# Optimization experiments

Hardware: AMD Instinct MI355X
Metric: run time of the kernel (lower is better)

The kernel has to match this reference:

```python
import jax, jax.numpy as jnp
import numpy as np


def _cell(x, ch_sum, cc_sum, W, b):
    # gates = W @ [child_h_sum, x] + b ; chunk order: f, i, c_tilde, o
    gates = jnp.concatenate([ch_sum, x], axis=-1) @ W.T + b
    f, i, ct, o = jnp.split(gates, 4, axis=-1)
    c = jax.nn.sigmoid(f) * cc_sum + jax.nn.sigmoid(i) * jnp.tanh(ct)
    h = jax.nn.sigmoid(o) * jnp.tanh(c)
    return h, c


def setup_inputs() -> dict:
    key = jax.random.key(0)
    k1, k2 = jax.random.split(key)
    H = 128                       # hidden_size == input_size (forced by recursion)
    L = 2 ** 17                   # num leaves of a perfect binary tree
    leaf_features = jax.random.normal(k1, (L, H), dtype=jnp.float32)
    lim = float(np.sqrt(6.0 / (2 * H + 4 * H)))  # xavier_uniform for (4H, 2H)
    W = jax.random.uniform(k2, (4 * H, 2 * H), minval=-lim, maxval=lim, dtype=jnp.float32)
    b = jnp.zeros((4 * H,), dtype=jnp.float32)
    return {"leaf_features": leaf_features, "W": W, "b": b}


def reference(leaf_features, W, b):
    H = W.shape[0] // 4
    L = leaf_features.shape[0]
    # Leaf level: no children -> child_h_sum = child_c_sum = 0
    zeros = jnp.zeros((L, H), dtype=leaf_features.dtype)
    h, c = _cell(leaf_features, zeros, zeros, W, b)
    # Internal levels (perfect binary tree), bottom-up. Loop count is static
    # (log2(L) levels), each iteration is fully vectorized over the level.
    while h.shape[0] > 1:
        hl, hr = h[0::2], h[1::2]
        cl, cr = c[0::2], c[1::2]
        ch_sum = hl + hr            # sum(child_h)
        x = ch_sum * 0.5            # child_h_avg (mean over 2 children)
        cc_sum = cl + cr            # summed child cell states
        h, c = _cell(x, ch_sum, cc_sum, W, b)
    return h  # root hidden state, shape (1, H)
```

## Files before the change

kernel.cpp:

```cpp
#include <hip/hip_runtime.h>

#define HH 128
#define NT 512
#define PT 256

typedef float  f32x4  __attribute__((ext_vector_type(4)));
typedef _Float16 f16x8 __attribute__((ext_vector_type(8)));

static __device__ __forceinline__ unsigned int pk16(float a, float b){
  unsigned short ha = __builtin_bit_cast(unsigned short, (_Float16)a);
  unsigned short hb = __builtin_bit_cast(unsigned short, (_Float16)b);
  return (unsigned int)ha | ((unsigned int)hb << 16);
}
static __device__ __forceinline__ float f16_to_f(unsigned short s){
  return (float)__builtin_bit_cast(_Float16, s);
}

__device__ __forceinline__ float sigf(float x){
  float t = __builtin_amdgcn_exp2f(-1.44269504089f * x);
  return __builtin_amdgcn_rcpf(1.f + t);
}
__device__ __forceinline__ float tanhf_(float x){
  float t = __builtin_amdgcn_exp2f(2.88539008178f * x);
  return 1.f - 2.f*__builtin_amdgcn_rcpf(t + 1.f);
}

__global__ __launch_bounds__(PT) void prep_pack(
    const float* __restrict__ W,
    unsigned short* __restrict__ pE, unsigned short* __restrict__ pL)
{
  int idx = blockIdx.x*PT + threadIdx.x;
  int l  = idx & 63;
  int kc = (idx >> 6) & 3;
  int gl = (idx >> 8) & 7;
  int wp = (idx >> 11);
  int q  = gl >> 1, ft = gl & 1;
  int g  = q*128 + wp*32 + ft*16 + (l & 15);
  int kbase = kc*32 + (l >> 4)*8;

  unsigned short ev[8], lv[8];
#pragma unroll
  for (int j = 0; j < 8; ++j){
    int k = kbase + j;
    float w0 = W[g*256 + k];
    float w1 = W[g*256 + 128 + k];
    float we = w0 + 0.5f*w1;
    ev[j] = __builtin_bit_cast(unsigned short, (_Float16)we);
    lv[j] = __builtin_bit_cast(unsigned short, (_Float16)w1);
  }
  long base = (long)idx*8;
  *(f16x8*)&pE[base] = *(f16x8*)ev;
  *(f16x8*)&pL[base] = *(f16x8*)lv;
}

__global__ __launch_bounds__(NT, 2) void leafK(
    const float* __restrict__ x_leaf,
    const unsigned short* __restrict__ pL,
    const float* __restrict__ bias,
    unsigned short* __restrict__ HpO,
    float* __restrict__ csO, int ntiles)
{
  __shared__ unsigned short AsH[2][32*HH];

  const int t = threadIdx.x, w = t>>6, l = t&63;
  const int a = l>>4, fcol = l&15, feat = w*16 + fcol;

  f16x8 rb[3][4];
#pragma unroll
  for (int qq = 0; qq < 3; ++qq)
#pragma unroll
    for (int kc = 0; kc < 4; ++kc){
      long off = ((long)((((w>>1)*8) + (qq+1)*2 + (w&1))*4 + kc)*64 + l)*8;
      rb[qq][kc] = *(const f16x8*)&pL[off];
    }
  const float Bi = bias[HH + feat], Bg = bias[2*HH + feat], Bo = bias[3*HH + feat];

  const int srow = t>>4, sci = t&15;
  float sv[8];
  auto sload = [&](int tile){
    long base = ((long)tile*32 + srow)*HH + sci*8;
    *(float4*)&sv[0] = *(const float4*)&x_leaf[base];
    *(float4*)&sv[4] = *(const float4*)&x_leaf[base+4];
  };
  auto swrite = [&](int buf){
    unsigned int hp[4];
#pragma unroll
    for (int p = 0; p < 4; ++p) hp[p] = pk16(sv[2*p], sv[2*p+1]);
    uint4 hq = {hp[0],hp[1],hp[2],hp[3]};
    int off = srow*256 + ((sci*16) ^ ((srow&7)<<4));
    *(uint4*)((char*)&AsH[buf][0] + off) = hq;
  };

  int tile = blockIdx.x;
  if (tile < ntiles){ sload(tile); swrite(0); }
  __syncthreads();
  int buf = 0;

  for (; tile < ntiles; tile += gridDim.x){
#pragma unroll
    for (int qq = 0; qq < 3; ++qq)
#pragma unroll
      for (int kc = 0; kc < 4; ++kc)
        asm volatile("" : "+v"(rb[qq][kc]));

    int nxt = tile + gridDim.x;
    bool have = nxt < ntiles;
    if (have) sload(nxt);

    f32x4 acc[2][3];
#pragma unroll
    for (int mt = 0; mt < 2; ++mt)
#pragma unroll
      for (int qq = 0; qq < 3; ++qq) acc[mt][qq] = (f32x4)(0.f);

#pragma unroll
    for (int kc = 0; kc < 4; ++kc){
      f16x8 aH[2];
#pragma unroll
      for (int mt = 0; mt < 2; ++mt){
        int row = mt*16 + fcol;
        int off = row*256 + ((kc*64 + a*16) ^ ((row&7)<<4));
        aH[mt] = *(const f16x8*)((const char*)&AsH[buf][0] + off);
      }
#pragma unroll
      for (int qq = 0; qq < 3; ++qq)
#pragma unroll
        for (int mt = 0; mt < 2; ++mt)
          acc[mt][qq] = __builtin_amdgcn_mfma_f32_16x16x32_f16(aH[mt], rb[qq][kc], acc[mt][qq], 0, 0, 0);
    }

#pragma unroll
    for (int mt = 0; mt < 2; ++mt){
      float hv[4], cv[4];
#pragma unroll
      for (int rr = 0; rr < 4; ++rr){
        float iv = acc[mt][0][rr] + Bi;
        float gv = acc[mt][1][rr] + Bg;
        float ov = acc[mt][2][rr] + Bo;
        float c = sigf(iv)*tanhf_(gv);
        float h = sigf(ov)*tanhf_(c);
        hv[rr] = h; cv[rr] = c;
      }
#pragma unroll
      for (int p = 0; p < 2; ++p){
        long prow = (long)tile*16 + mt*8 + a*2 + p;
        float hs = hv[2*p] + hv[2*p+1];
        HpO[prow*HH + feat] = __builtin_bit_cast(unsigned short, (_Float16)hs);
        csO[prow*HH + feat] = cv[2*p] + cv[2*p+1];
      }
    }

    if (have) swrite(buf^1);
    __syncthreads();
    buf ^= 1;
  }
}

__global__ __launch_bounds__(NT, 2) void fuse2(
    const unsigned short* __restrict__ hPH,
    const float* __restrict__ cP,
    const unsigned short* __restrict__ pE,
    const float* __restrict__ bias,
    unsigned short* __restrict__ HpO,
    float* __restrict__ csO, int ntiles)
{
  __shared__ unsigned short AsH[2][32*HH];
  __shared__ float HsF[16*HH];
  __shared__ float CsF[16*HH];

  const int t = threadIdx.x, w = t>>6, l = t&63;
  const int a = l>>4, fcol = l&15, feat = w*16 + fcol;

  f16x8 rb[4][4];
#pragma unroll
  for (int q = 0; q < 4; ++q)
#pragma unroll
    for (int kc = 0; kc < 4; ++kc){
      long off = ((long)((((w>>1)*8) + q*2 + (w&1))*4 + kc)*64 + l)*8;
      rb[q][kc] = *(const f16x8*)&pE[off];
    }
  float B4[4];
#pragma unroll
  for (int q = 0; q < 4; ++q) B4[q] = bias[q*HH + feat];

  const int srow = t>>4, sci = t&15;
  f16x8 svH;
  auto sload = [&](int tile){
    long base = ((long)tile*32 + srow)*HH + sci*8;
    svH = *(const f16x8*)&hPH[base];
  };
  auto swrite = [&](int buf){
    int off = srow*256 + ((sci*16) ^ ((srow&7)<<4));
    *(f16x8*)((char*)&AsH[buf][0] + off) = svH;
  };

  int tile = blockIdx.x;
  if (tile < ntiles){ sload(tile); swrite(0); }
  __syncthreads();
  int buf = 0;

  for (; tile < ntiles; tile += gridDim.x){
#pragma unroll
    for (int q = 0; q < 4; ++q)
#pragma unroll
      for (int kc = 0; kc < 4; ++kc)
        asm volatile("" : "+v"(rb[q][kc]));

    int nxt = tile + gridDim.x;
    bool have = nxt < ntiles;

    float cc0[2][4];
#pragma unroll
    for (int mt = 0; mt < 2; ++mt)
#pragma unroll
      for (int rr = 0; rr < 4; ++rr)
        cc0[mt][rr] = cP[((long)tile*32 + mt*16 + a*4 + rr)*HH + feat];

    if (have) sload(nxt);

    f32x4 acc0[2][4];
#pragma unroll
    for (int mt = 0; mt < 2; ++mt)
#pragma unroll
      for (int q = 0; q < 4; ++q) acc0[mt][q] = (f32x4)(0.f);

#pragma unroll
    for (int kc = 0; kc < 4; ++kc){
      f16x8 aH[2];
#pragma unroll
      for (int mt = 0; mt < 2; ++mt){
        int row = mt*16 + fcol;
        int off = row*256 + ((kc*64 + a*16) ^ ((row&7)<<4));
        aH[mt] = *(const f16x8*)((const char*)&AsH[buf][0] + off);
      }
#pragma unroll
      for (int q = 0; q < 4; ++q)
#pragma unroll
        for (int mt = 0; mt < 2; ++mt)
          acc0[mt][q] = __builtin_amdgcn_mfma_f32_16x16x32_f16(aH[mt], rb[q][kc], acc0[mt][q], 0, 0, 0);
    }

#pragma unroll
    for (int mt = 0; mt < 2; ++mt){
      float hv[4], cv[4];
#pragma unroll
      for (int rr = 0; rr < 4; ++rr){
        float fv = acc0[mt][0][rr] + B4[0];
        float iv = acc0[mt][1][rr] + B4[1];
        float gv = acc0[mt][2][rr] + B4[2];
        float ov = acc0[mt][3][rr] + B4[3];
        float c = sigf(fv)*cc0[mt][rr] + sigf(iv)*tanhf_(gv);
        float h = sigf(ov)*tanhf_(c);
        hv[rr] = h; cv[rr] = c;
      }
#pragma unroll
      for (int p = 0; p < 2; ++p){
        int row1 = mt*8 + a*2 + p;
        int o1 = row1*512 + ((feat*4) ^ ((row1&7)<<4));
        *(float*)((char*)HsF + o1) = hv[2*p] + hv[2*p+1];
        *(float*)((char*)CsF + o1) = cv[2*p] + cv[2*p+1];
      }
    }
    if (have) swrite(buf^1);
    __syncthreads();

    f32x4 acc1[4];
#pragma unroll
    for (int q = 0; q < 4; ++q) acc1[q] = (f32x4)(0.f);

#pragma unroll
    for (int kc = 0; kc < 4; ++kc){
      f16x8 a1H;
      {
        int cb = kc*128 + a*32;
        const char* base = (const char*)HsF + fcol*512;
        float av[8];
        *(float4*)&av[0] = *(const float4*)(base + ( cb       ^ ((fcol&7)<<4)));
        *(float4*)&av[4] = *(const float4*)(base + ((cb + 16) ^ ((fcol&7)<<4)));
        unsigned int hp[4];
#pragma unroll
        for (int p = 0; p < 4; ++p) hp[p] = pk16(av[2*p], av[2*p+1]);
        uint4 hq = {hp[0],hp[1],hp[2],hp[3]};
        a1H = *(f16x8*)&hq;
      }
#pragma unroll
      for (int q = 0; q < 4; ++q)
        acc1[q] = __builtin_amdgcn_mfma_f32_16x16x32_f16(a1H, rb[q][kc], acc1[q], 0, 0, 0);
    }

    {
      float hv[4], cv[4];
#pragma unroll
      for (int rr = 0; rr < 4; ++rr){
        int n = a*4 + rr;
        float ccv = *(const float*)((const char*)CsF + n*512 + ((feat*4) ^ ((n&7)<<4)));
        float fv = acc1[0][rr] + B4[0];
        float iv = acc1[1][rr] + B4[1];
        float gv = acc1[2][rr] + B4[2];
        float ov = acc1[3][rr] + B4[3];
        float c = sigf(fv)*ccv + sigf(iv)*tanhf_(gv);
        float h = sigf(ov)*tanhf_(c);
        hv[rr] = h; cv[rr] = c;
      }
#pragma unroll
      for (int p = 0; p < 2; ++p){
        long prow = (long)tile*8 + a*2 + p;
        float hs = hv[2*p] + hv[2*p+1];
        HpO[prow*HH + feat] = __builtin_bit_cast(unsigned short, (_Float16)hs);
        csO[prow*HH + feat] = cv[2*p] + cv[2*p+1];
      }
    }
    __syncthreads();
    buf ^= 1;
  }
}

template<int ROWS0, int NLEV, int INPLANES, int FINAL>
__global__ __launch_bounds__(NT, 2) void treeblk2(
    const unsigned short* __restrict__ Hp,
    const float* __restrict__ cs,
    const float* __restrict__ hraw, const float* __restrict__ craw,
    const unsigned short* __restrict__ pE,
    const float* __restrict__ bias,
    float* __restrict__ h_out, float* __restrict__ c_out,
    float* __restrict__ root_out)
{
  constexpr int MT = (ROWS0 >= 16) ? (ROWS0/16) : 1;
  __shared__ float Asum[ROWS0][132];
  __shared__ float Csum[ROWS0][132];

  const int t = threadIdx.x;
  const long blk = blockIdx.x;
  const int w = t >> 6, l = t & 63;
  const int a = l >> 4, fcol = l & 15, feat = w*16 + fcol;

  {
    constexpr int EPT = ROWS0*HH/NT;
    constexpr int TPR = HH/EPT;
    int row = t/TPR, c0 = (t%TPR)*EPT;
    if (INPLANES){
      long base = (blk*ROWS0 + row)*(long)HH + c0;
#pragma unroll
      for (int j = 0; j < EPT; ++j){
        Asum[row][c0+j] = f16_to_f(Hp[base+j]);
        Csum[row][c0+j] = cs[base+j];
      }
    } else {
      long g = (blk*2*ROWS0 + 2*row)*(long)HH + c0;
#pragma unroll
      for (int j = 0; j < EPT; ++j){
        Asum[row][c0+j] = hraw[g+j] + hraw[g+HH+j];
        Csum[row][c0+j] = craw[g+j] + craw[g+HH+j];
      }
    }
  }

  f16x8 rb[4][4];
#pragma unroll
  for (int q = 0; q < 4; ++q)
#pragma unroll
    for (int kc = 0; kc < 4; ++kc){
      long off = ((long)((((w>>1)*8) + q*2 + (w&1))*4 + kc)*64 + l)*8;
      rb[q][kc] = *(const f16x8*)&pE[off];
    }
  float B4[4];
#pragma unroll
  for (int q = 0; q < 4; ++q) B4[q] = bias[q*HH + feat];

  __syncthreads();

#pragma unroll
  for (int lv = 0; lv < NLEV; ++lv){
    const int rows  = ROWS0 >> lv;
    const int tiles = (rows >= 16) ? (rows/16) : 1;
    float hv[MT][4], cv[MT][4];

#pragma unroll
    for (int mt = 0; mt < MT; ++mt){
      if (mt >= tiles) continue;
      f16x8 aH[4];
#pragma unroll
      for (int kc = 0; kc < 4; ++kc){
        const float* ap = &Asum[mt*16 + fcol][kc*32 + a*8];
        float av[8];
        *(float4*)&av[0] = *(const float4*)&ap[0];
        *(float4*)&av[4] = *(const float4*)&ap[4];
        unsigned int hp[4];
#pragma unroll
        for (int p = 0; p < 4; ++p) hp[p] = pk16(av[2*p], av[2*p+1]);
        uint4 hq = {hp[0],hp[1],hp[2],hp[3]};
        aH[kc] = *(f16x8*)&hq;
      }
      f32x4 acc[4];
#pragma unroll
      for (int q = 0; q < 4; ++q) acc[q] = (f32x4)(0.f);
#pragma unroll
      for (int kc = 0; kc < 4; ++kc){
#pragma unroll
        for (int q = 0; q < 4; ++q)
          acc[q] = __builtin_amdgcn_mfma_f32_16x16x32_f16(aH[kc], rb[q][kc], acc[q], 0, 0, 0);
      }
#pragma unroll
      for (int rr = 0; rr < 4; ++rr){
        int n = mt*16 + a*4 + rr;
        float ccv = Csum[n][feat];
        float fv = acc[0][rr] + B4[0];
        float iv = acc[1][rr] + B4[1];
        float gv = acc[2][rr] + B4[2];
        float ov = acc[3][rr] + B4[3];
        float c = sigf(fv)*ccv + sigf(iv)*tanhf_(gv);
        float h = sigf(ov)*tanhf_(c);
        hv[mt][rr] = h; cv[mt][rr] = c;
      }
    }
    __syncthreads();

    if (lv < NLEV-1){
#pragma unroll
      for (int mt = 0; mt < MT; ++mt){
        if (mt >= tiles) continue;
#pragma unroll
        for (int p = 0; p < 2; ++p){
          int n0 = mt*16 + a*4 + 2*p;
          if (n0 < rows){
            int prow = n0 >> 1;
            Asum[prow][feat] = hv[mt][2*p] + hv[mt][2*p+1];
            Csum[prow][feat] = cv[mt][2*p] + cv[mt][2*p+1];
          }
        }
      }
      __syncthreads();
    } else if (FINAL){
      if (a == 0) root_out[feat] = hv[0][0];
    } else {
      if (a == 0){
        h_out[blk*HH + feat] = hv[0][0];
        c_out[blk*HH + feat] = cv[0][0];
      }
    }
  }
}

extern "C" void kernel_launch(void* const* d_in, const int* in_sizes, int n_in,
                              void* d_out, int out_size, void* d_ws, size_t ws_size,
                              hipStream_t stream){
  const float* leaf = (const float*)d_in[0];
  const float* W    = (const float*)d_in[1];
  const float* bias = (const float*)d_in[2];
  float* out = (float*)d_out;

  unsigned short* pE  = (unsigned short*)d_ws;
  unsigned short* pL  = pE + 65536;
  unsigned short* HpA = pL + 65536;
  unsigned short* HpB = HpA + (1l<<16)*HH;
  float* csA = (float*)(HpB + (1l<<14)*HH);
  float* csB = csA + (1l<<16)*HH;
  float* h32 = csB + (1l<<14)*HH;
  float* c32 = h32 + 32*HH;

  prep_pack<<<32, PT, 0, stream>>>(W, pE, pL);

  leafK<<<512, NT, 0, stream>>>(leaf, pL, bias, HpA, csA, 4096);
  fuse2<<<512, NT, 0, stream>>>(HpA, csA, pE, bias, HpB, csB, 2048);
  fuse2<<<256, NT, 0, stream>>>(HpB, csB, pE, bias, HpA, csA, 512);
  fuse2<<<128, NT, 0, stream>>>(HpA, csA, pE, bias, HpB, csB, 128);
  treeblk2<32,6,1,0><<<32, NT, 0, stream>>>(HpB, csB, nullptr, nullptr,
                                            pE, bias, h32, c32, nullptr);
  treeblk2<16,5,0,1><<<1, NT, 0, stream>>>(nullptr, nullptr, h32, c32,
                                           pE, bias, nullptr, nullptr, out);

  (void)in_sizes; (void)n_in; (void)out_size; (void)ws_size;
}
```

Measured before the change: 95.92 us.

## Fuse first internal tree level into leaf kernel and store hidden sums as fp16

The leaf kernel now computes the next tree level in the same pass. It stages the pair-summed h and c in shared memory and runs a second MFMA GEMM with the combined internal weights, which halves the intermediate written to global memory and removes one level from the later kernels. The shared hidden-sum staging in both leaf and fuse kernels becomes fp16, so the MMA operand is read directly without float-to-half repacking. The launch chain and workspace sizes shift down a level, and the final tree kernel is adapted for 8-row inputs padded to 16. In exchange the leaf kernel holds more weight registers, which may pressure occupancy.

New measurement: 98.86 us. 3.1% more time.

```diff
diff --git a/kernel.cpp b/kernel.cpp
--- a/kernel.cpp
+++ b/kernel.cpp
@@ -53,27 +53,38 @@
   *(f16x8*)&pL[base] = *(f16x8*)lv;
 }
 
-__global__ __launch_bounds__(NT, 2) void leafK(
+__global__ __launch_bounds__(NT, 2) void leaf2(
     const float* __restrict__ x_leaf,
-    const unsigned short* __restrict__ pL,
+    const unsigned short* __restrict__ pL, const unsigned short* __restrict__ pE,
     const float* __restrict__ bias,
     unsigned short* __restrict__ HpO,
     float* __restrict__ csO, int ntiles)
 {
   __shared__ unsigned short AsH[2][32*HH];
+  __shared__ unsigned short HsF[16*HH];
+  __shared__ float          CsF[16*HH];
 
   const int t = threadIdx.x, w = t>>6, l = t&63;
   const int a = l>>4, fcol = l&15, feat = w*16 + fcol;
 
-  f16x8 rb[3][4];
+  f16x8 rb0[3][4], rb1[4][4];
 #pragma unroll
   for (int qq = 0; qq < 3; ++qq)
 #pragma unroll
     for (int kc = 0; kc < 4; ++kc){
       long off = ((long)((((w>>1)*8) + (qq+1)*2 + (w&1))*4 + kc)*64 + l)*8;
-      rb[qq][kc] = *(const f16x8*)&pL[off];
-    }
-  const float Bi = bias[HH + feat], Bg = bias[2*HH + feat], Bo = bias[3*HH + feat];
+      rb0[qq][kc] = *(const f16x8*)&pL[off];
+    }
+#pragma unroll
+  for (int q = 0; q < 4; ++q)
+#pragma unroll
+    for (int kc = 0; kc < 4; ++kc){
+      long off = ((long)((((w>>1)*8) + q*2 + (w&1))*4 + kc)*64 + l)*8;
+      rb1[q][kc] = *(const f16x8*)&pE[off];
+    }
+  float B4[4];
+#pragma unroll
+  for (int q = 0; q < 4; ++q) B4[q] = bias[q*HH + feat];
 
   const int srow = t>>4, sci = t&15;
   float sv[8];
@@ -101,17 +112,22 @@
     for (int qq = 0; qq < 3; ++qq)
 #pragma unroll
       for (int kc = 0; kc < 4; ++kc)
-        asm volatile("" : "+v"(rb[qq][kc]));
+        asm volatile("" : "+v"(rb0[qq][kc]));
+#pragma unroll
+    for (int q = 0; q < 4; ++q)
+#pragma unroll
+      for (int kc = 0; kc < 4; ++kc)
+        asm volatile("" : "+v"(rb1[q][kc]));
 
     int nxt = tile + gridDim.x;
     bool have = nxt < ntiles;
     if (have) sload(nxt);
 
-    f32x4 acc[2][3];
+    f32x4 acc0[2][3];
 #pragma unroll
     for (int mt = 0; mt < 2; ++mt)
 #pragma unroll
-      for (int qq = 0; qq < 3; ++qq) acc[mt][qq] = (f32x4)(0.f);
+      for (int qq = 0; qq < 3; ++qq) acc0[mt][qq] = (f32x4)(0.f);
 
 #pragma unroll
     for (int kc = 0; kc < 4; ++kc){
@@ -126,7 +142,7 @@
       for (int qq = 0; qq < 3; ++qq)
 #pragma unroll
         for (int mt = 0; mt < 2; ++mt)
-          acc[mt][qq] = __builtin_amdgcn_mfma_f32_16x16x32_f16(aH[mt], rb[qq][kc], acc[mt][qq], 0, 0, 0);
+          acc0[mt][qq] = __builtin_amdgcn_mfma_f32_16x16x32_f16(aH[mt], rb0[qq][kc], acc0[mt][qq], 0, 0, 0);
     }
 
 #pragma unroll
@@ -134,23 +150,60 @@
       float hv[4], cv[4];
 #pragma unroll
       for (int rr = 0; rr < 4; ++rr){
-        float iv = acc[mt][0][rr] + Bi;
-        float gv = acc[mt][1][rr] + Bg;
-        float ov = acc[mt][2][rr] + Bo;
+        float iv = acc0[mt][0][rr] + B4[1];
+        float gv = acc0[mt][1][rr] + B4[2];
+        float ov = acc0[mt][2][rr] + B4[3];
         float c = sigf(iv)*tanhf_(gv);
         float h = sigf(ov)*tanhf_(c);
         hv[rr] = h; cv[rr] = c;
       }
 #pragma unroll
       for (int p = 0; p < 2; ++p){
-        long prow = (long)tile*16 + mt*8 + a*2 + p;
+        int row1 = mt*8 + a*2 + p;
+        float hs = hv[2*p] + hv[2*p+1];
+        *(unsigned short*)((char*)HsF + row1*256 + ((feat*2) ^ ((row1&7)<<4))) =
+            __builtin_bit_cast(unsigned short, (_Float16)hs);
+        *(float*)((char*)CsF + row1*512 + ((feat*4) ^ ((row1&7)<<4))) =
+            cv[2*p] + cv[2*p+1];
+      }
+    }
+    if (have) swrite(buf^1);
+    __syncthreads();
+
+    f32x4 acc1[4];
+#pragma unroll
+    for (int q = 0; q < 4; ++q) acc1[q] = (f32x4)(0.f);
+#pragma unroll
+    for (int kc = 0; kc < 4; ++kc){
+      int off = fcol*256 + ((kc*64 + a*16) ^ ((fcol&7)<<4));
+      f16x8 a1H = *(const f16x8*)((const char*)HsF + off);
+#pragma unroll
+      for (int q = 0; q < 4; ++q)
+        acc1[q] = __builtin_amdgcn_mfma_f32_16x16x32_f16(a1H, rb1[q][kc], acc1[q], 0, 0, 0);
+    }
+
+    {
+      float hv[4], cv[4];
+#pragma unroll
+      for (int rr = 0; rr < 4; ++rr){
+        int n = a*4 + rr;
+        float ccv = *(const float*)((const char*)CsF + n*512 + ((feat*4) ^ ((n&7)<<4)));
+        float fv = acc1[0][rr] + B4[0];
+        float iv = acc1[1][rr] + B4[1];
+        float gv = acc1[2][rr] + B4[2];
+        float ov = acc1[3][rr] + B4[3];
+        float c = sigf(fv)*ccv + sigf(iv)*tanhf_(gv);
+        float h = sigf(ov)*tanhf_(c);
+        hv[rr] = h; cv[rr] = c;
+      }
+#pragma unroll
+      for (int p = 0; p < 2; ++p){
+        long prow = (long)tile*8 + a*2 + p;
         float hs = hv[2*p] + hv[2*p+1];
         HpO[prow*HH + feat] = __builtin_bit_cast(unsigned short, (_Float16)hs);
         csO[prow*HH + feat] = cv[2*p] + cv[2*p+1];
       }
     }
-
-    if (have) swrite(buf^1);
     __syncthreads();
     buf ^= 1;
   }
@@ -165,8 +218,8 @@
     float* __restrict__ csO, int ntiles)
 {
   __shared__ unsigned short AsH[2][32*HH];
-  __shared__ float HsF[16*HH];
-  __shared__ float CsF[16*HH];
+  __shared__ unsigned short HsF[16*HH];
+  __shared__ float          CsF[16*HH];
 
   const int t = threadIdx.x, w = t>>6, l = t&63;
   const int a = l>>4, fcol = l&15, feat = w*16 + fcol;
@@ -256,9 +309,11 @@
 #pragma unroll
       for (int p = 0; p < 2; ++p){
         int row1 = mt*8 + a*2 + p;
-        int o1 = row1*512 + ((feat*4) ^ ((row1&7)<<4));
-        *(float*)((char*)HsF + o1) = hv[2*p] + hv[2*p+1];
-        *(float*)((char*)CsF + o1) = cv[2*p] + cv[2*p+1];
+        float hs = hv[2*p] + hv[2*p+1];
+        *(unsigned short*)((char*)HsF + row1*256 + ((feat*2) ^ ((row1&7)<<4))) =
+            __builtin_bit_cast(unsigned short, (_Float16)hs);
+        *(float*)((char*)CsF + row1*512 + ((feat*4) ^ ((row1&7)<<4))) =
+            cv[2*p] + cv[2*p+1];
       }
     }
     if (have) swrite(buf^1);
@@ -267,22 +322,10 @@
     f32x4 acc1[4];
 #pragma unroll
     for (int q = 0; q < 4; ++q) acc1[q] = (f32x4)(0.f);
-
-#pragma unroll
-    for (int kc = 0; kc < 4; ++kc){
-      f16x8 a1H;
-      {
-        int cb = kc*128 + a*32;
-        const char* base = (const char*)HsF + fcol*512;
-        float av[8];
-        *(float4*)&av[0] = *(const float4*)(base + ( cb       ^ ((fcol&7)<<4)));
-        *(float4*)&av[4] = *(const float4*)(base + ((cb + 16) ^ ((fcol&7)<<4)));
-        unsigned int hp[4];
-#pragma unroll
-        for (int p = 0; p < 4; ++p) hp[p] = pk16(av[2*p], av[2*p+1]);
-        uint4 hq = {hp[0],hp[1],hp[2],hp[3]};
-        a1H = *(f16x8*)&hq;
-      }
+#pragma unroll
+    for (int kc = 0; kc < 4; ++kc){
+      int off = fcol*256 + ((kc*64 + a*16) ^ ((fcol&7)<<4));
+      f16x8 a1H = *(const f16x8*)((const char*)HsF + off);
 #pragma unroll
       for (int q = 0; q < 4; ++q)
         acc1[q] = __builtin_amdgcn_mfma_f32_16x16x32_f16(a1H, rb[q][kc], acc1[q], 0, 0, 0);
@@ -326,8 +369,9 @@
     float* __restrict__ root_out)
 {
   constexpr int MT = (ROWS0 >= 16) ? (ROWS0/16) : 1;
-  __shared__ float Asum[ROWS0][132];
-  __shared__ float Csum[ROWS0][132];
+  constexpr int AR = (ROWS0 < 16) ? 16 : ROWS0;
+  __shared__ float Asum[AR][132];
+  __shared__ float Csum[AR][132];
 
   const int t = threadIdx.x;
   const long blk = blockIdx.x;
@@ -351,6 +395,16 @@
       for (int j = 0; j < EPT; ++j){
         Asum[row][c0+j] = hraw[g+j] + hraw[g+HH+j];
         Csum[row][c0+j] = craw[g+j] + craw[g+HH+j];
+      }
+    }
+    if (ROWS0 < 16){
+      int prow2 = ROWS0 + row;
+      if (prow2 < 16){
+#pragma unroll
+        for (int j = 0; j < EPT; ++j){
+          Asum[prow2][c0+j] = 0.f;
+          Csum[prow2][c0+j] = 0.f;
+        }
       }
     }
   }
@@ -452,22 +506,22 @@
   unsigned short* pE  = (unsigned short*)d_ws;
   unsigned short* pL  = pE + 65536;
   unsigned short* HpA = pL + 65536;
-  unsigned short* HpB = HpA + (1l<<16)*HH;
-  float* csA = (float*)(HpB + (1l<<14)*HH);
-  float* csB = csA + (1l<<16)*HH;
-  float* h32 = csB + (1l<<14)*HH;
-  float* c32 = h32 + 32*HH;
+  unsigned short* HpB = HpA + (1l<<15)*HH;
+  float* csA = (float*)(HpB + (1l<<13)*HH);
+  float* csB = csA + (1l<<15)*HH;
+  float* h16 = csB + (1l<<13)*HH;
+  float* c16 = h16 + 16*HH;
 
   prep_pack<<<32, PT, 0, stream>>>(W, pE, pL);
 
-  leafK<<<512, NT, 0, stream>>>(leaf, pL, bias, HpA, csA, 4096);
-  fuse2<<<512, NT, 0, stream>>>(HpA, csA, pE, bias, HpB, csB, 2048);
-  fuse2<<<256, NT, 0, stream>>>(HpB, csB, pE, bias, HpA, csA, 512);
-  fuse2<<<128, NT, 0, stream>>>(HpA, csA, pE, bias, HpB, csB, 128);
-  treeblk2<32,6,1,0><<<32, NT, 0, stream>>>(HpB, csB, nullptr, nullptr,
-                                            pE, bias, h32, c32, nullptr);
-  treeblk2<16,5,0,1><<<1, NT, 0, stream>>>(nullptr, nullptr, h32, c32,
-                                           pE, bias, nullptr, nullptr, out);
+  leaf2<<<512, NT, 0, stream>>>(leaf, pL, pE, bias, HpA, csA, 4096);
+  fuse2<<<512, NT, 0, stream>>>(HpA, csA, pE, bias, HpB, csB, 1024);
+  fuse2<<<256, NT, 0, stream>>>(HpB, csB, pE, bias, HpA, csA, 256);
+  fuse2<<<64, NT, 0, stream>>>(HpA, csA, pE, bias, HpB, csB, 64);
+  treeblk2<32,6,1,0><<<16, NT, 0, stream>>>(HpB, csB, nullptr, nullptr,
+                                            pE, bias, h16, c16, nullptr);
+  treeblk2<8,4,0,1><<<1, NT, 0, stream>>>(nullptr, nullptr, h16, c16,
+                                          pE, bias, nullptr, nullptr, out);
 
   (void)in_sizes; (void)n_in; (void)out_size; (void)ws_size;
 }
```
